# Performance work log

Hardware: AMD Instinct MI355X
Metric: run time of the kernel (lower is better)

## Reference

```python
import jax, jax.numpy as jnp
import numpy as np

def _round_ste(x):
    # StraightThrough: forward = round, backward = identity
    return x + jax.lax.stop_gradient(jnp.round(x) - x)

def setup_inputs() -> dict:
    key = jax.random.key(0)
    k1, k2, k3, k4, k5 = jax.random.split(key, 5)
    in_f, out_f, n_tok = 4096, 4096, 8192
    return {
        "input": jax.random.normal(k1, (n_tok, in_f), dtype=jnp.float32),
        "weight": jax.random.normal(k2, (out_f, in_f), dtype=jnp.float32),
        "bias": jax.random.normal(k3, (out_f,), dtype=jnp.float32),
        "w_scale": jax.random.uniform(k4, (1,), dtype=jnp.float32),
        "b_scale": jax.random.uniform(k5, (1,), dtype=jnp.float32),
    }

def reference(input, weight, bias, w_scale, b_scale):
    # straight-through rounding of quantized latents (use_straight_through=True, compress_bias=True)
    w_q = _round_ste(weight)
    b_q = _round_ste(bias)
    # decoder: per-tensor affine dequantization
    w_dec = w_scale * w_q          # [out, in]
    b_dec = b_scale * b_q          # [out]
    # F.linear: input @ weight.T + bias
    return jnp.einsum('ni,oi->no', input, w_dec) + b_dec
```

## Files before the change

kernel.cpp:

```cpp
#include <hip/hip_runtime.h>
#include <stdint.h>


using bf16x8   = __attribute__((ext_vector_type(8))) __bf16;
using floatx16 = __attribute__((ext_vector_type(16))) float;
using us8      = __attribute__((ext_vector_type(8))) unsigned short;
using us4      = __attribute__((ext_vector_type(4))) unsigned short;

__device__ __forceinline__ unsigned short f2bf_rne(float x) {
    unsigned int u = __float_as_uint(x);
    return (unsigned short)((u + 0x7fffu + ((u >> 16) & 1u)) >> 16);
}

__device__ __forceinline__ void stage16(const unsigned short* g, unsigned short* l) {
    __builtin_amdgcn_global_load_lds(
        (__attribute__((address_space(1))) void*)g,
        (__attribute__((address_space(3))) void*)l,
        16, 0, 0);
}

__global__ __launch_bounds__(256) void cvt_both(
    const float* __restrict__ inA, unsigned short* __restrict__ outA, long long nA4,
    const float* __restrict__ inB, unsigned short* __restrict__ outB, long long nB4) {
    const long long i = (long long)blockIdx.x * 256 + threadIdx.x;
    if (i < nA4) {
        float4 v = ((const float4*)inA)[i];
        us4 o = { f2bf_rne(v.x), f2bf_rne(v.y), f2bf_rne(v.z), f2bf_rne(v.w) };
        ((us4*)outA)[i] = o;
    } else {
        const long long j = i - nA4;
        if (j < nB4) {
            float4 v = ((const float4*)inB)[j];
            us4 o = { f2bf_rne(rintf(v.x)), f2bf_rne(rintf(v.y)),
                      f2bf_rne(rintf(v.z)), f2bf_rne(rintf(v.w)) };
            ((us4*)outB)[j] = o;
        }
    }
}

__global__ __launch_bounds__(512) void gemm256_ph(
    const unsigned short* __restrict__ A,
    const unsigned short* __restrict__ B,
    const float* __restrict__ bias,
    const float* __restrict__ wscale_p,
    const float* __restrict__ bscale_p,
    float* __restrict__ C,
    int M, int N, int K) {
    constexpr int BK   = 64;
    constexpr int TILE = 256 * BK;
    __shared__ unsigned short ldsA[2 * TILE];
    __shared__ unsigned short ldsB[2 * TILE];

    const int tid  = threadIdx.x;
    const int wave = tid >> 6;
    const int lane = tid & 63;

    const int nbx = N >> 8;
    int wg;
    {
        const int cpx = (int)gridDim.x >> 3;
        wg = ((int)blockIdx.x & 7) * cpx + ((int)blockIdx.x >> 3);
    }
    const int bm = (wg / nbx) << 8;
    const int bn = (wg % nbx) << 8;

    const int wm    = (wave >> 2) << 7;
    const int wn    = (wave & 3) << 6;
    const int col   = lane & 31;
    const int khalf = lane >> 5;

    const int row512 = tid >> 3;
    const int gk = ((tid & 7) ^ (row512 & 7)) << 3;
    const unsigned short* gA = A + (size_t)(bm + row512) * K + gk;
    const unsigned short* gB = B + (size_t)(bn + row512) * K + gk;
    unsigned short* sA = ldsA + (wave << 9);
    unsigned short* sB = ldsB + (wave << 9);

    int rowA[4], rowB[2], slotv[4];
#pragma unroll
    for (int mi = 0; mi < 4; ++mi) rowA[mi] = (wm + mi * 32 + col) << 6;
#pragma unroll
    for (int ni = 0; ni < 2; ++ni) rowB[ni] = (wn + ni * 32 + col) << 6;
#pragma unroll
    for (int ks = 0; ks < 4; ++ks) slotv[ks] = ((ks * 2 + khalf) ^ (col & 7)) << 3;

    const float wsc = wscale_p[0];
    const float bsc = bscale_p[0];
    float badd[2];
#pragma unroll
    for (int ni = 0; ni < 2; ++ni)
        badd[ni] = bsc * rintf(bias[bn + wn + ni * 32 + col]);

    const int NT = K >> 6;

    stage16(gA,                     sA);
    stage16(gA + (size_t)128 * K,   sA + 2 * 4096);
    stage16(gB,                     sB);
    stage16(gB + (size_t)64 * K,    sB + 1 * 4096);
    stage16(gB + (size_t)128 * K,   sB + 2 * 4096);
    stage16(gB + (size_t)192 * K,   sB + 3 * 4096);
    stage16(gA + (size_t)64 * K,    sA + 1 * 4096);
    stage16(gA + (size_t)192 * K,   sA + 3 * 4096);
    asm volatile("s_waitcnt vmcnt(2)" ::: "memory");
    __builtin_amdgcn_s_barrier();
    __builtin_amdgcn_sched_barrier(0);

    floatx16 acc[4][2] = {};

#define LDA_F(mi, ks) __builtin_bit_cast(bf16x8, *(const us8*)&SA[rowA[mi] + slotv[ks]])
#define LDB_F(ni, ks) __builtin_bit_cast(bf16x8, *(const us8*)&SB[rowB[ni] + slotv[ks]])

#define PH_BAR_LGKM()                                        \
    __builtin_amdgcn_s_barrier();                            \
    asm volatile("s_waitcnt lgkmcnt(0)" ::: "memory");       \
    __builtin_amdgcn_sched_barrier(0);

#define PH_MFMA(MIB, KSB)                                                     \
    __builtin_amdgcn_s_setprio(1);                                            \
    _Pragma("unroll") for (int k2 = 0; k2 < 2; ++k2)                          \
        _Pragma("unroll") for (int m2 = 0; m2 < 2; ++m2)                      \
            _Pragma("unroll") for (int ni = 0; ni < 2; ++ni)                  \
                acc[(MIB) + m2][ni] = __builtin_amdgcn_mfma_f32_32x32x16_bf16(\
                    Af[m2][k2], Bf[ni][(KSB) + k2], acc[(MIB) + m2][ni],      \
                    0, 0, 0);                                                 \
    __builtin_amdgcn_s_setprio(0);                                            \
    __builtin_amdgcn_sched_barrier(0);

    for (int t = 0; t < NT; ++t) {
        const unsigned short* SA = ldsA + (t & 1) * TILE;
        const unsigned short* SB = ldsB + (t & 1) * TILE;
        unsigned short* dA = sA + ((t + 1) & 1) * TILE;
        unsigned short* dB = sB + ((t + 1) & 1) * TILE;
        const size_t kt1 = (size_t)(t + 1) * BK;
        const bool st = (t + 1 < NT);

        bf16x8 Af[2][2];
        bf16x8 Bf[2][4];

#pragma unroll
        for (int m2 = 0; m2 < 2; ++m2)
#pragma unroll
            for (int k2 = 0; k2 < 2; ++k2) Af[m2][k2] = LDA_F(m2, k2);
#pragma unroll
        for (int ni = 0; ni < 2; ++ni)
#pragma unroll
            for (int k2 = 0; k2 < 2; ++k2) Bf[ni][k2] = LDB_F(ni, k2);
        if (st) {
            stage16(gA + kt1,                   dA);
            stage16(gA + (size_t)128 * K + kt1, dA + 2 * 4096);
            stage16(gB + kt1,                   dB);
            stage16(gB + (size_t)64 * K + kt1,  dB + 1 * 4096);
        }
        PH_BAR_LGKM()
        PH_MFMA(0, 0)
        __builtin_amdgcn_s_barrier();
        __builtin_amdgcn_sched_barrier(0);

#pragma unroll
        for (int m2 = 0; m2 < 2; ++m2)
#pragma unroll
            for (int k2 = 0; k2 < 2; ++k2) Af[m2][k2] = LDA_F(m2, 2 + k2);
#pragma unroll
        for (int ni = 0; ni < 2; ++ni)
#pragma unroll
            for (int k2 = 0; k2 < 2; ++k2) Bf[ni][2 + k2] = LDB_F(ni, 2 + k2);
        if (st) {
            stage16(gB + (size_t)128 * K + kt1, dB + 2 * 4096);
            stage16(gB + (size_t)192 * K + kt1, dB + 3 * 4096);
        }
        PH_BAR_LGKM()
        PH_MFMA(0, 2)
        asm volatile("s_waitcnt vmcnt(6)" ::: "memory");
        __builtin_amdgcn_s_barrier();
        __builtin_amdgcn_sched_barrier(0);

#pragma unroll
        for (int m2 = 0; m2 < 2; ++m2)
#pragma unroll
            for (int k2 = 0; k2 < 2; ++k2) Af[m2][k2] = LDA_F(2 + m2, k2);
        PH_BAR_LGKM()
        PH_MFMA(2, 0)
        __builtin_amdgcn_s_barrier();
        __builtin_amdgcn_sched_barrier(0);

#pragma unroll
        for (int m2 = 0; m2 < 2; ++m2)
#pragma unroll
            for (int k2 = 0; k2 < 2; ++k2) Af[m2][k2] = LDA_F(2 + m2, 2 + k2);
        if (st) {
            stage16(gA + (size_t)64 * K + kt1,  dA + 1 * 4096);
            stage16(gA + (size_t)192 * K + kt1, dA + 3 * 4096);
        }
        PH_BAR_LGKM()
        PH_MFMA(2, 2)
        asm volatile("s_waitcnt vmcnt(2)" ::: "memory");
        __builtin_amdgcn_s_barrier();
        __builtin_amdgcn_sched_barrier(0);
    }

#undef LDA_F
#undef LDB_F
#undef PH_BAR_LGKM
#undef PH_MFMA

    const int rb = khalf << 2;
#pragma unroll
    for (int mi = 0; mi < 4; ++mi) {
#pragma unroll
        for (int ni = 0; ni < 2; ++ni) {
            const int n = bn + wn + ni * 32 + col;
#pragma unroll
            for (int reg = 0; reg < 16; ++reg) {
                const int m = bm + wm + mi * 32 + (reg & 3) + 8 * (reg >> 2) + rb;
                C[(size_t)m * N + n] = acc[mi][ni][reg] * wsc + badd[ni];
            }
        }
    }
}

__global__ __launch_bounds__(256) void gemm_bf16_bt(
    const unsigned short* __restrict__ A,
    const unsigned short* __restrict__ B,
    const float* __restrict__ bias,
    const float* __restrict__ wscale_p,
    const float* __restrict__ bscale_p,
    float* __restrict__ C,
    int M, int N, int K) {
    constexpr int BM = 128, BK = 64;
    __shared__ unsigned short ldsA[BM * BK];
    __shared__ unsigned short ldsB[BM * BK];

    const int tid  = threadIdx.x;
    const int wave = tid >> 6;
    const int lane = tid & 63;

    const int bm = blockIdx.y * BM;
    const int bn = blockIdx.x * BM;
    const int wm = (wave >> 1) * 64;
    const int wn = (wave & 1) * 64;

    const float wsc = wscale_p[0];
    const float bsc = bscale_p[0];

    const int col = lane & 31;
    const int khalf = lane >> 5;

    float badd[2];
#pragma unroll
    for (int ni = 0; ni < 2; ++ni)
        badd[ni] = bsc * rintf(bias[bn + wn + ni * 32 + col]);

    const int g_st = ((lane & 7) ^ (lane >> 3)) * 8;
    const unsigned short* gAp[4];
    const unsigned short* gBp[4];
    unsigned short* lA[4];
    unsigned short* lB[4];
#pragma unroll
    for (int i = 0; i < 4; ++i) {
        const int r = wave * 32 + i * 8 + (lane >> 3);
        gAp[i] = A + (size_t)(bm + r) * K + g_st;
        gBp[i] = B + (size_t)(bn + r) * K + g_st;
        lA[i] = &ldsA[(wave * 256 + i * 64) * 8];
        lB[i] = &ldsB[(wave * 256 + i * 64) * 8];
    }

    floatx16 acc[2][2] = {};

    for (int kt = 0; kt < K; kt += BK) {
#pragma unroll
        for (int i = 0; i < 4; ++i) {
            stage16(gAp[i] + kt, lA[i]);
            stage16(gBp[i] + kt, lB[i]);
        }
        __syncthreads();

#pragma unroll
        for (int ks = 0; ks < 4; ++ks) {
            const int gc = ks * 2 + khalf;
            const int slot = (gc ^ (lane & 7)) * 8;
            bf16x8 af[2], bfr[2];
#pragma unroll
            for (int mi = 0; mi < 2; ++mi) {
                const int off = (wm + mi * 32 + col) * BK + slot;
                af[mi] = __builtin_bit_cast(bf16x8, *(const us8*)&ldsA[off]);
            }
#pragma unroll
            for (int ni = 0; ni < 2; ++ni) {
                const int off = (wn + ni * 32 + col) * BK + slot;
                bfr[ni] = __builtin_bit_cast(bf16x8, *(const us8*)&ldsB[off]);
            }
#pragma unroll
            for (int mi = 0; mi < 2; ++mi)
#pragma unroll
                for (int ni = 0; ni < 2; ++ni)
                    acc[mi][ni] = __builtin_amdgcn_mfma_f32_32x32x16_bf16(
                        af[mi], bfr[ni], acc[mi][ni], 0, 0, 0);
        }
        __syncthreads();
    }

    const int rbase = 4 * khalf;
#pragma unroll
    for (int mi = 0; mi < 2; ++mi) {
#pragma unroll
        for (int ni = 0; ni < 2; ++ni) {
            const int n = bn + wn + ni * 32 + col;
#pragma unroll
            for (int reg = 0; reg < 16; ++reg) {
                const int m = bm + wm + mi * 32 + (reg & 3) + 8 * (reg >> 2) + rbase;
                C[(size_t)m * N + n] = acc[mi][ni][reg] * wsc + badd[ni];
            }
        }
    }
}

__global__ __launch_bounds__(256) void fallback_gemm(
    const float* __restrict__ A, const float* __restrict__ W,
    const float* __restrict__ bias, const float* __restrict__ wsp,
    const float* __restrict__ bsp, float* __restrict__ C, int M, int N, int K) {
    const int n = blockIdx.x * 256 + threadIdx.x;
    const int m = blockIdx.y;
    if (n >= N || m >= M) return;
    float s = 0.f;
    for (int k = 0; k < K; ++k)
        s += A[(size_t)m * K + k] * rintf(W[(size_t)n * K + k]);
    C[(size_t)m * N + n] = s * wsp[0] + bsp[0] * rintf(bias[n]);
}

extern "C" void kernel_launch(void* const* d_in, const int* in_sizes, int n_in,
                              void* d_out, int out_size, void* d_ws, size_t ws_size,
                              hipStream_t stream) {
    const float* input  = (const float*)d_in[0];
    const float* weight = (const float*)d_in[1];
    const float* bias   = (const float*)d_in[2];
    const float* wscale = (const float*)d_in[3];
    const float* bscale = (const float*)d_in[4];
    float* out = (float*)d_out;

    const int N = in_sizes[2];
    const int K = in_sizes[1] / N;
    const int M = in_sizes[0] / K;

    const size_t needA = (size_t)M * K * sizeof(unsigned short);
    const size_t needB = (size_t)N * K * sizeof(unsigned short);

    if (ws_size >= needA + needB && (M % 128) == 0 && (N % 128) == 0 &&
        (K % 64) == 0) {
        unsigned short* Abf = (unsigned short*)d_ws;
        unsigned short* Bbf = (unsigned short*)((char*)d_ws + needA);
        const long long nA4 = (long long)M * K / 4;
        const long long nB4 = (long long)N * K / 4;
        const long long nthr = nA4 + nB4;
        cvt_both<<<(unsigned)((nthr + 255) / 256), 256, 0, stream>>>(
            input, Abf, nA4, weight, Bbf, nB4);

        const int nwg256 = (M / 256) * (N / 256);
        if ((M % 256) == 0 && (N % 256) == 0 && (K / 64) >= 4 &&
            (nwg256 % 8) == 0) {
            gemm256_ph<<<dim3(nwg256), 512, 0, stream>>>(
                Abf, Bbf, bias, wscale, bscale, out, M, N, K);
        } else {
            dim3 grid(N / 128, M / 128);
            gemm_bf16_bt<<<grid, 256, 0, stream>>>(Abf, Bbf, bias, wscale,
                                                   bscale, out, M, N, K);
        }
    } else {
        dim3 grid((N + 255) / 256, M);
        fallback_gemm<<<grid, 256, 0, stream>>>(input, weight, bias, wscale, bscale, out, M, N, K);
    }
}
```

Before: 551.0 us.

## Stage GEMM tiles into LDS in MFMA fragment-major layout

Changes the LDS layout of the A and B tiles from row-major with an XOR swizzle to a fragment-major layout. Each 32x16 MFMA operand block is stored contiguously, so a wave reads its fragment with one linear per-lane 16-byte read and no swizzle arithmetic. The global-to-LDS staging is remapped so each wave loads whole fragment blocks, and the tail iterations now guard their vmcnt waits. Global loads now cover 32 rows by 16 bf16 elements per instruction rather than full 128-byte row segments, which may reduce global coalescing in exchange for conflict-free LDS reads.

```diff
diff --git a/kernel.cpp b/kernel.cpp
--- a/kernel.cpp
+++ b/kernel.cpp
@@ -38,7 +38,7 @@
     }
 }
 
-__global__ __launch_bounds__(512) void gemm256_ph(
+__global__ __launch_bounds__(512) void gemm256_fm(
     const unsigned short* __restrict__ A,
     const unsigned short* __restrict__ B,
     const float* __restrict__ bias,
@@ -47,7 +47,7 @@
     float* __restrict__ C,
     int M, int N, int K) {
     constexpr int BK   = 64;
-    constexpr int TILE = 256 * BK;
+    constexpr int TILE = 16384;
     __shared__ unsigned short ldsA[2 * TILE];
     __shared__ unsigned short ldsB[2 * TILE];
 
@@ -64,51 +64,52 @@
     const int bm = (wg / nbx) << 8;
     const int bn = (wg % nbx) << 8;
 
-    const int wm    = (wave >> 2) << 7;
-    const int wn    = (wave & 3) << 6;
+    const int wr    = wave >> 2;
+    const int wc    = wave & 3;
     const int col   = lane & 31;
     const int khalf = lane >> 5;
 
-    const int row512 = tid >> 3;
-    const int gk = ((tid & 7) ^ (row512 & 7)) << 3;
-    const unsigned short* gA = A + (size_t)(bm + row512) * K + gk;
-    const unsigned short* gB = B + (size_t)(bn + row512) * K + gk;
-    unsigned short* sA = ldsA + (wave << 9);
-    unsigned short* sB = ldsB + (wave << 9);
-
-    int rowA[4], rowB[2], slotv[4];
-#pragma unroll
-    for (int mi = 0; mi < 4; ++mi) rowA[mi] = (wm + mi * 32 + col) << 6;
-#pragma unroll
-    for (int ni = 0; ni < 2; ++ni) rowB[ni] = (wn + ni * 32 + col) << 6;
-#pragma unroll
-    for (int ks = 0; ks < 4; ++ks) slotv[ks] = ((ks * 2 + khalf) ^ (col & 7)) << 3;
+    const int q   = wave >> 1;
+    const int mb1 = (q & 1) + ((q >> 1) << 2);
+    const int mb3 = mb1 + 2;
+    const int kb  = (wave & 1) << 1;
+
+    const unsigned short* gAl = A + (size_t)(bm + col) * K + (khalf << 3);
+    const unsigned short* gBl = B + (size_t)(bn + col) * K + (khalf << 3);
+
+    const int lane16 = lane << 3;
 
     const float wsc = wscale_p[0];
     const float bsc = bscale_p[0];
     float badd[2];
 #pragma unroll
     for (int ni = 0; ni < 2; ++ni)
-        badd[ni] = bsc * rintf(bias[bn + wn + ni * 32 + col]);
+        badd[ni] = bsc * rintf(bias[bn + wc * 64 + ni * 32 + col]);
 
     const int NT = K >> 6;
 
-    stage16(gA,                     sA);
-    stage16(gA + (size_t)128 * K,   sA + 2 * 4096);
-    stage16(gB,                     sB);
-    stage16(gB + (size_t)64 * K,    sB + 1 * 4096);
-    stage16(gB + (size_t)128 * K,   sB + 2 * 4096);
-    stage16(gB + (size_t)192 * K,   sB + 3 * 4096);
-    stage16(gA + (size_t)64 * K,    sA + 1 * 4096);
-    stage16(gA + (size_t)192 * K,   sA + 3 * 4096);
+#define ABLK(buf, mb, ks) ((buf) * TILE + (((mb) * 4 + (ks)) << 9))
+#define BBLK(buf, nb, ks) ((buf) * TILE + (((nb) * 4 + (ks)) << 9))
+#define ST_A(buf, mb, ks, kt) \
+    stage16(gAl + (size_t)((mb) * 32) * K + (kt) + (ks) * 16, &ldsA[ABLK(buf, mb, ks)])
+#define ST_B(buf, nb, ks, kt) \
+    stage16(gBl + (size_t)((nb) * 32) * K + (kt) + (ks) * 16, &ldsB[BBLK(buf, nb, ks)])
+#define RD_A(buf, mb, ks) \
+    __builtin_bit_cast(bf16x8, *(const us8*)&ldsA[ABLK(buf, mb, ks) + lane16])
+#define RD_B(buf, nb, ks) \
+    __builtin_bit_cast(bf16x8, *(const us8*)&ldsB[BBLK(buf, nb, ks) + lane16])
+
+#pragma unroll
+    for (int i = 0; i < 4; ++i) ST_B(0, wave, i, 0);
+    ST_A(0, mb1, kb, 0);
+    ST_A(0, mb1, kb + 1, 0);
+    ST_A(0, mb3, kb, 0);
+    ST_A(0, mb3, kb + 1, 0);
     asm volatile("s_waitcnt vmcnt(2)" ::: "memory");
     __builtin_amdgcn_s_barrier();
     __builtin_amdgcn_sched_barrier(0);
 
     floatx16 acc[4][2] = {};
-
-#define LDA_F(mi, ks) __builtin_bit_cast(bf16x8, *(const us8*)&SA[rowA[mi] + slotv[ks]])
-#define LDB_F(ni, ks) __builtin_bit_cast(bf16x8, *(const us8*)&SB[rowB[ni] + slotv[ks]])
 
 #define PH_BAR_LGKM()                                        \
     __builtin_amdgcn_s_barrier();                            \
@@ -127,11 +128,9 @@
     __builtin_amdgcn_sched_barrier(0);
 
     for (int t = 0; t < NT; ++t) {
-        const unsigned short* SA = ldsA + (t & 1) * TILE;
-        const unsigned short* SB = ldsB + (t & 1) * TILE;
-        unsigned short* dA = sA + ((t + 1) & 1) * TILE;
-        unsigned short* dB = sB + ((t + 1) & 1) * TILE;
-        const size_t kt1 = (size_t)(t + 1) * BK;
+        const int rb_ = t & 1;
+        const int sb_ = (t + 1) & 1;
+        const int kt1 = (t + 1) * BK;
         const bool st = (t + 1 < NT);
 
         bf16x8 Af[2][2];
@@ -140,16 +139,14 @@
 #pragma unroll
         for (int m2 = 0; m2 < 2; ++m2)
 #pragma unroll
-            for (int k2 = 0; k2 < 2; ++k2) Af[m2][k2] = LDA_F(m2, k2);
+            for (int k2 = 0; k2 < 2; ++k2) Af[m2][k2] = RD_A(rb_, wr * 4 + m2, k2);
 #pragma unroll
         for (int ni = 0; ni < 2; ++ni)
 #pragma unroll
-            for (int k2 = 0; k2 < 2; ++k2) Bf[ni][k2] = LDB_F(ni, k2);
+            for (int k2 = 0; k2 < 2; ++k2) Bf[ni][k2] = RD_B(rb_, wc * 2 + ni, k2);
         if (st) {
-            stage16(gA + kt1,                   dA);
-            stage16(gA + (size_t)128 * K + kt1, dA + 2 * 4096);
-            stage16(gB + kt1,                   dB);
-            stage16(gB + (size_t)64 * K + kt1,  dB + 1 * 4096);
+#pragma unroll
+            for (int i = 0; i < 4; ++i) ST_B(sb_, wave, i, kt1);
         }
         PH_BAR_LGKM()
         PH_MFMA(0, 0)
@@ -159,25 +156,26 @@
 #pragma unroll
         for (int m2 = 0; m2 < 2; ++m2)
 #pragma unroll
-            for (int k2 = 0; k2 < 2; ++k2) Af[m2][k2] = LDA_F(m2, 2 + k2);
+            for (int k2 = 0; k2 < 2; ++k2) Af[m2][k2] = RD_A(rb_, wr * 4 + m2, 2 + k2);
 #pragma unroll
         for (int ni = 0; ni < 2; ++ni)
 #pragma unroll
-            for (int k2 = 0; k2 < 2; ++k2) Bf[ni][2 + k2] = LDB_F(ni, 2 + k2);
+            for (int k2 = 0; k2 < 2; ++k2) Bf[ni][2 + k2] = RD_B(rb_, wc * 2 + ni, 2 + k2);
         if (st) {
-            stage16(gB + (size_t)128 * K + kt1, dB + 2 * 4096);
-            stage16(gB + (size_t)192 * K + kt1, dB + 3 * 4096);
+            ST_A(sb_, mb1, kb, kt1);
+            ST_A(sb_, mb1, kb + 1, kt1);
         }
         PH_BAR_LGKM()
         PH_MFMA(0, 2)
-        asm volatile("s_waitcnt vmcnt(6)" ::: "memory");
+        if (st) { asm volatile("s_waitcnt vmcnt(6)" ::: "memory"); }
+        else    { asm volatile("s_waitcnt vmcnt(0)" ::: "memory"); }
         __builtin_amdgcn_s_barrier();
         __builtin_amdgcn_sched_barrier(0);
 
 #pragma unroll
         for (int m2 = 0; m2 < 2; ++m2)
 #pragma unroll
-            for (int k2 = 0; k2 < 2; ++k2) Af[m2][k2] = LDA_F(2 + m2, k2);
+            for (int k2 = 0; k2 < 2; ++k2) Af[m2][k2] = RD_A(rb_, wr * 4 + 2 + m2, k2);
         PH_BAR_LGKM()
         PH_MFMA(2, 0)
         __builtin_amdgcn_s_barrier();
@@ -186,32 +184,36 @@
 #pragma unroll
         for (int m2 = 0; m2 < 2; ++m2)
 #pragma unroll
-            for (int k2 = 0; k2 < 2; ++k2) Af[m2][k2] = LDA_F(2 + m2, 2 + k2);
+            for (int k2 = 0; k2 < 2; ++k2) Af[m2][k2] = RD_A(rb_, wr * 4 + 2 + m2, 2 + k2);
         if (st) {
-            stage16(gA + (size_t)64 * K + kt1,  dA + 1 * 4096);
-            stage16(gA + (size_t)192 * K + kt1, dA + 3 * 4096);
+            ST_A(sb_, mb3, kb, kt1);
+            ST_A(sb_, mb3, kb + 1, kt1);
         }
         PH_BAR_LGKM()
         PH_MFMA(2, 2)
-        asm volatile("s_waitcnt vmcnt(2)" ::: "memory");
+        if (st) { asm volatile("s_waitcnt vmcnt(2)" ::: "memory"); }
         __builtin_amdgcn_s_barrier();
         __builtin_amdgcn_sched_barrier(0);
     }
 
-#undef LDA_F
-#undef LDB_F
 #undef PH_BAR_LGKM
 #undef PH_MFMA
+#undef ABLK
+#undef BBLK
+#undef ST_A
+#undef ST_B
+#undef RD_A
+#undef RD_B
 
     const int rb = khalf << 2;
 #pragma unroll
     for (int mi = 0; mi < 4; ++mi) {
 #pragma unroll
         for (int ni = 0; ni < 2; ++ni) {
-            const int n = bn + wn + ni * 32 + col;
+            const int n = bn + wc * 64 + ni * 32 + col;
 #pragma unroll
             for (int reg = 0; reg < 16; ++reg) {
-                const int m = bm + wm + mi * 32 + (reg & 3) + 8 * (reg >> 2) + rb;
+                const int m = bm + wr * 128 + mi * 32 + (reg & 3) + 8 * (reg >> 2) + rb;
                 C[(size_t)m * N + n] = acc[mi][ni][reg] * wsc + badd[ni];
             }
         }
@@ -355,9 +357,9 @@
             input, Abf, nA4, weight, Bbf, nB4);
 
         const int nwg256 = (M / 256) * (N / 256);
-        if ((M % 256) == 0 && (N % 256) == 0 && (K / 64) >= 4 &&
+        if ((M % 256) == 0 && (N % 256) == 0 && (K / 64) >= 1 &&
             (nwg256 % 8) == 0) {
-            gemm256_ph<<<dim3(nwg256), 512, 0, stream>>>(
+            gemm256_fm<<<dim3(nwg256), 512, 0, stream>>>(
                 Abf, Bbf, bias, wscale, bscale, out, M, N, K);
         } else {
             dim3 grid(N / 128, M / 128);
```

Measured after the change: 630.7 us. 14.5% more time.
